# Optimization experiments

Measured on AMD Instinct MI355X. Metric: run time of the kernel, lower is better.

The kernel has to match this reference:

```python
import jax, jax.numpy as jnp
import numpy as np

B, C, H, W = 4, 256, 96, 96
HEADS, RATE = 8, 1


def setup_inputs() -> dict:
    key = jax.random.key(0)
    ks = [jax.random.fold_in(key, i) for i in range(8)]
    kpe = 2 * (RATE // 2) + 1  # PE depthwise kernel size (1 for rate=1)
    return {
        "q": jax.random.normal(ks[0], (B, C, H, W), jnp.float32),
        "k": jax.random.normal(ks[1], (B, C, H, W), jnp.float32),
        "v": jax.random.normal(ks[2], (B, C, H, W), jnp.float32),
        "wq": jax.random.normal(ks[3], (C, C), jnp.float32) * 0.02,          # q_proj 1x1 (used for q,k,v per source)
        "pe_dw": jax.random.normal(ks[4], (9, 1, kpe, kpe), jnp.float32) * 0.3,  # grouped conv, groups=9
        "pe_pw": jax.random.normal(ks[5], (9, 9, 1, 1), jnp.float32) * 0.3,      # 1x1 mixing conv
        "wo": jax.random.normal(ks[6], (C, C), jnp.float32) * 0.02,          # out_proj weight
        "bo": jax.random.normal(ks[7], (C,), jnp.float32) * 0.02,            # out_proj bias
    }


def _unfold3(x, rate):
    # torch.nn.Unfold(3, dilation=rate, padding=rate) then view(N, c, 9, H, W)
    # kernel positions are row-major (ki, kj), channel-major layout -> stack on axis 2.
    n, c, h, w = x.shape
    xp = jnp.pad(x, ((0, 0), (0, 0), (rate, rate), (rate, rate)))
    pats = [xp[:, :, i * rate:i * rate + h, j * rate:j * rate + w]
            for i in range(3) for j in range(3)]
    return jnp.stack(pats, axis=2)  # (N, c, 9, H, W)


def reference(q, b_unused_k=None, v=None, wq=None, pe_dw=None, pe_pw=None, wo=None, bo=None, k=None):
    raise NotImplementedError  # replaced below


def reference(q, k, v, wq, pe_dw, pe_pw, wo, bo):
    b = q.shape[0]
    ch = C // HEADS
    proj = lambda x: jnp.einsum('oc,bchw->bohw', wq, x)  # source uses q_proj for q, k AND v
    qh = proj(q).reshape(b * HEADS, ch, H, W)
    kh = proj(k).reshape(b * HEADS, ch, H, W)
    vh = proj(v).reshape(b * HEADS, ch, H, W)

    ku = _unfold3(kh, RATE)                              # (bH, ch, 9, H, W)
    f = jnp.einsum('nchw,nckhw->nkhw', qh, ku)           # per-pixel 3x3 scores (bH, 9, H, W)

    pad = RATE // 2
    dn = ('NCHW', 'OIHW', 'NCHW')
    f = jax.lax.conv_general_dilated(f, pe_dw, (1, 1), [(pad, pad), (pad, pad)],
                                     feature_group_count=9, dimension_numbers=dn)
    f = jax.lax.conv_general_dilated(f, pe_pw, (1, 1), 'VALID', dimension_numbers=dn)
    s = jax.nn.softmax(f, axis=1)                        # softmax over 9 kernel positions

    vu = _unfold3(vh, RATE)                              # (bH, ch, 9, H, W)
    o = jnp.einsum('nckhw,nkhw->nchw', vu, s).reshape(b, C, H, W)
    return jnp.einsum('oc,bchw->bohw', wo, o) + bo[None, :, None, None]
```

## Files before the change

### kernel.cpp

```cpp
#include <hip/hip_runtime.h>
#include <math.h>

#define HH 96
#define WW 96
#define PP 9216
#define CCH 256
#define BB 4
#define CH 32

typedef unsigned short u16;
typedef short bf16x8 __attribute__((ext_vector_type(8)));
typedef float f32x4 __attribute__((ext_vector_type(4)));

__device__ __forceinline__ float bf2f(unsigned s) { return __uint_as_float(s << 16); }
__device__ __forceinline__ u16 f2bf(float f) {
  unsigned u = __float_as_uint(f);
  return (u16)((u + 0x7fffu + ((u >> 16) & 1u)) >> 16);
}

typedef __attribute__((address_space(1))) const unsigned int GUI;
typedef __attribute__((address_space(3))) unsigned int LUI;
__device__ __forceinline__ void gload16(const void* g, void* l) {
  __builtin_amdgcn_global_load_lds((GUI*)g, (LUI*)l, 16, 0, 0);
}

__global__ __launch_bounds__(256)
void wcvt(const float* __restrict__ wq, const float* __restrict__ wo,
          u16* __restrict__ Wbf) {
  int gidx = blockIdx.x * 256 + threadIdx.x;
  int mat = gidx >> 13;
  int gi = gidx & 8191;
  int l = gi & 63;
  int i = (gi >> 6) & 3;
  int w = (gi >> 8) & 3;
  int ks = (gi >> 10) & 1;
  int kk = (gi >> 11) & 3;
  const float* W = mat ? wo : wq;
  int row = w * 64 + i * 16 + (l & 15);
  int c0 = kk * 64 + (ks * 4 + (l >> 4)) * 8;
  const float* s = W + (size_t)row * CCH + c0;
  float4 a = *(const float4*)s;
  float4 b = *(const float4*)(s + 4);
  uint4 u;
  u.x = (unsigned)f2bf(a.x) | ((unsigned)f2bf(a.y) << 16);
  u.y = (unsigned)f2bf(a.z) | ((unsigned)f2bf(a.w) << 16);
  u.z = (unsigned)f2bf(b.x) | ((unsigned)f2bf(b.y) << 16);
  u.w = (unsigned)f2bf(b.z) | ((unsigned)f2bf(b.w) << 16);
  *(uint4*)(Wbf + (size_t)gidx * 8) = u;
}

#define XROW 264
__global__ __launch_bounds__(512, 6)
void gemm_qkvf(const float* __restrict__ qin, const float* __restrict__ kin,
               const float* __restrict__ vin, const u16* __restrict__ Wbf,
               u16* __restrict__ Xcl) {
  __shared__ u16 Xb[64 * XROW];
  const int t = threadIdx.x;
  const int w = t >> 6, l = t & 63;
  const int lr = l & 15, lg = l >> 4;
  const int pblk = blockIdx.x * 64;
  const int z = blockIdx.z;
  const int b = z & 3, which = z >> 2;
  const float* Xf = ((which == 0) ? qin : (which == 1) ? kin : vin) + (size_t)b * CCH * PP;
  u16* Y = Xcl + (size_t)z * ((size_t)PP * CCH);

  float4 xr[8];
#pragma unroll
  for (int rr = 0; rr < 8; rr++) {
    int cc = w * 32 + rr * 4 + lg;
    xr[rr] = *(const float4*)(Xf + (size_t)cc * PP + pblk + lr * 4);
  }
#pragma unroll
  for (int rr = 0; rr < 8; rr++) {
    float r0 = xr[rr].x, r1 = xr[rr].y, r2 = xr[rr].z, r3 = xr[rr].w;
    bool b0 = (lg & 1), b1 = (lg & 2);
    float s0 = b0 ? r0 : r1;
    float s1 = b0 ? r2 : r3;
    float u0 = __shfl_xor(s0, 16, 64);
    float u1 = __shfl_xor(s1, 16, 64);
    float m0 = b0 ? u0 : r0;
    float m1 = b0 ? r1 : u0;
    float m2 = b0 ? u1 : r2;
    float m3 = b0 ? r3 : u1;
    float s2 = b1 ? m0 : m2;
    float s3 = b1 ? m1 : m3;
    float w0 = __shfl_xor(s2, 32, 64);
    float w1 = __shfl_xor(s3, 32, 64);
    float o0 = b1 ? w0 : m0;
    float o1 = b1 ? w1 : m1;
    float o2 = b1 ? m2 : w0;
    float o3 = b1 ? m3 : w1;
    int cbase = w * 32 + rr * 4;
    int pl = lr * 4 + lg;
    unsigned lo = (unsigned)f2bf(o0) | ((unsigned)f2bf(o1) << 16);
    unsigned hi = (unsigned)f2bf(o2) | ((unsigned)f2bf(o3) << 16);
    *(uint2*)(&Xb[pl * XROW + cbase]) = make_uint2(lo, hi);
  }
  __syncthreads();

  f32x4 acc[2][4];
#pragma unroll
  for (int mi = 0; mi < 2; mi++)
#pragma unroll
    for (int ni = 0; ni < 4; ni++) acc[mi][ni] = (f32x4){0.f, 0.f, 0.f, 0.f};

#pragma unroll
  for (int kk = 0; kk < 4; kk++)
#pragma unroll
    for (int ks = 0; ks < 2; ks++) {
      const int q = kk * 8 + ks * 4 + lg;
      bf16x8 wf[2], xf[4];
#pragma unroll
      for (int mi = 0; mi < 2; mi++) {
        size_t go = ((((size_t)(kk * 2 + ks) * 4 + (w >> 1)) * 4 +
                      ((w & 1) * 2 + mi)) * 64 + l) * 8;
        wf[mi] = *(const bf16x8*)(Wbf + go);
      }
#pragma unroll
      for (int i = 0; i < 4; i++) {
        int row = i * 16 + lr;
        xf[i] = *(const bf16x8*)&Xb[row * XROW + q * 8];
      }
#pragma unroll
      for (int mi = 0; mi < 2; mi++)
#pragma unroll
        for (int ni = 0; ni < 4; ni++)
          acc[mi][ni] = __builtin_amdgcn_mfma_f32_16x16x32_bf16(
              wf[mi], xf[ni], acc[mi][ni], 0, 0, 0);
    }

#pragma unroll
  for (int mi = 0; mi < 2; mi++)
#pragma unroll
    for (int ni = 0; ni < 4; ni++) {
      int o = w * 32 + mi * 16 + lg * 4;
      int p = pblk + ni * 16 + lr;
      f32x4 a = acc[mi][ni];
      uint2 u;
      u.x = (unsigned)f2bf(a[0]) | ((unsigned)f2bf(a[1]) << 16);
      u.y = (unsigned)f2bf(a[2]) | ((unsigned)f2bf(a[3]) << 16);
      *(uint2*)(Y + (size_t)p * CCH + o) = u;
    }
}

__global__ __launch_bounds__(256)
void gemm_out_m(const u16* __restrict__ Xbuf, const u16* __restrict__ Wbf,
                const float* __restrict__ bias, float* __restrict__ outY) {
  __shared__ u16 Xl[64 * 256];
  const int t = threadIdx.x;
  const int w = t >> 6, l = t & 63;
  const int lr = l & 15, lg = l >> 4;
  const int pblk = blockIdx.x * 64;
  const int z = blockIdx.z;
  const u16* Xb = Xbuf + (size_t)z * ((size_t)PP * CCH);

#pragma unroll
  for (int r = 0; r < 8; r++) {
    int G = r * 256 + t;
    int row = G >> 5, g = G & 31;
    int gs = (g & 24) | ((g & 7) ^ (row & 7));
    gload16(Xb + (size_t)(pblk + row) * CCH + gs * 8, (void*)&Xl[(size_t)G * 8]);
  }
  __syncthreads();

  f32x4 acc[4][4];
#pragma unroll
  for (int mi = 0; mi < 4; mi++)
#pragma unroll
    for (int ni = 0; ni < 4; ni++) acc[mi][ni] = (f32x4){0.f, 0.f, 0.f, 0.f};

#pragma unroll
  for (int kk = 0; kk < 4; kk++)
#pragma unroll
    for (int ks = 0; ks < 2; ks++) {
      const int q = kk * 8 + ks * 4 + lg;
      bf16x8 wf[4], xf[4];
#pragma unroll
      for (int i = 0; i < 4; i++) {
        size_t go = ((((size_t)(kk * 2 + ks) * 4 + w) * 4 + i) * 64 + l) * 8;
        wf[i] = *(const bf16x8*)(Wbf + go);
      }
#pragma unroll
      for (int i = 0; i < 4; i++) {
        int row = i * 16 + lr;
        int qp = (q & 24) | ((q & 7) ^ (row & 7));
        xf[i] = *(const bf16x8*)&Xl[row * 256 + qp * 8];
      }
#pragma unroll
      for (int mi = 0; mi < 4; mi++)
#pragma unroll
        for (int ni = 0; ni < 4; ni++)
          acc[mi][ni] = __builtin_amdgcn_mfma_f32_16x16x32_bf16(
              xf[mi], wf[ni], acc[mi][ni], 0, 0, 0);
    }

#pragma unroll
  for (int ni = 0; ni < 4; ni++) {
    int o = w * 64 + ni * 16 + lr;
    float bv = bias[o];
#pragma unroll
    for (int mi = 0; mi < 4; mi++) {
      int p = pblk + mi * 16 + lg * 4;
      f32x4 a = acc[mi][ni];
      float4 st = {a[0] + bv, a[1] + bv, a[2] + bv, a[3] + bv};
      *(float4*)(outY + ((size_t)z * CCH + o) * PP + p) = st;
    }
  }
}

#define TX 32
#define TY 4
#define HX 34
#define HY 6
#define NHP (HX * HY)
#define NGR (NHP * 4)
#define ARND 4

__device__ __forceinline__ void fma8(const uint4 u, const float* qp, float& s) {
  s = fmaf(qp[0], bf2f(u.x & 0xffffu), s);
  s = fmaf(qp[1], bf2f(u.x >> 16), s);
  s = fmaf(qp[2], bf2f(u.y & 0xffffu), s);
  s = fmaf(qp[3], bf2f(u.y >> 16), s);
  s = fmaf(qp[4], bf2f(u.z & 0xffffu), s);
  s = fmaf(qp[5], bf2f(u.z >> 16), s);
  s = fmaf(qp[6], bf2f(u.w & 0xffffu), s);
  s = fmaf(qp[7], bf2f(u.w >> 16), s);
}
__device__ __forceinline__ void acc8(const uint4 u, float gv, float* op) {
  op[0] = fmaf(gv, bf2f(u.x & 0xffffu), op[0]);
  op[1] = fmaf(gv, bf2f(u.x >> 16), op[1]);
  op[2] = fmaf(gv, bf2f(u.y & 0xffffu), op[2]);
  op[3] = fmaf(gv, bf2f(u.y >> 16), op[3]);
  op[4] = fmaf(gv, bf2f(u.z & 0xffffu), op[4]);
  op[5] = fmaf(gv, bf2f(u.z >> 16), op[5]);
  op[6] = fmaf(gv, bf2f(u.w & 0xffffu), op[6]);
  op[7] = fmaf(gv, bf2f(u.w >> 16), op[7]);
}

__global__ __launch_bounds__(256)
void attn_1b(const u16* __restrict__ Kt, const u16* __restrict__ Vt,
             u16* __restrict__ Qt, const float* __restrict__ pe_dw,
             const float* __restrict__ pe_pw) {
  __shared__ __align__(16) u16 kl[NHP * 32];
  __shared__ __align__(16) u16 vl[NHP * 32];
  __shared__ float coef[81];
  const int t = threadIdx.x;
  if (t < 81) coef[t] = pe_pw[t] * pe_dw[t % 9];

  const int lx = t & 31;
  const int h2 = (t >> 5) & 1;
  const int ly = t >> 6;
  const int x0 = blockIdx.x * TX;
  const int y0 = blockIdx.y * TY;
  const int b = blockIdx.z >> 3;
  const int h = blockIdx.z & 7;
  const size_t nbase = (size_t)b * PP * CCH + h * CH;
  const int p = (y0 + ly) * WW + (x0 + lx);
  const size_t pixhalf = nbase + (size_t)p * CCH + h2 * 16;

  uint4 kg[ARND], vg[ARND];
#pragma unroll
  for (int r = 0; r < ARND; r++) {
    int s = t + r * 256;
    int pix = s >> 2, g = s & 3;
    int hy = pix / HX, hx = pix - hy * HX;
    int gx = x0 - 1 + hx, gy = y0 - 1 + hy;
    bool ok = (s < NGR) & (gx >= 0) & (gx < WW) & (gy >= 0) & (gy < HH);
    uint4 u = make_uint4(0u, 0u, 0u, 0u);
    if (ok) u = *(const uint4*)(Kt + nbase + (size_t)(gy * WW + gx) * CCH + g * 8);
    kg[r] = u;
  }
#pragma unroll
  for (int r = 0; r < ARND; r++) {
    int s = t + r * 256;
    int pix = s >> 2, g = s & 3;
    int hy = pix / HX, hx = pix - hy * HX;
    int gx = x0 - 1 + hx, gy = y0 - 1 + hy;
    bool ok = (s < NGR) & (gx >= 0) & (gx < WW) & (gy >= 0) & (gy < HH);
    uint4 u = make_uint4(0u, 0u, 0u, 0u);
    if (ok) u = *(const uint4*)(Vt + nbase + (size_t)(gy * WW + gx) * CCH + g * 8);
    vg[r] = u;
  }
  uint4 q0 = *(const uint4*)(Qt + pixhalf);
  uint4 q1 = *(const uint4*)(Qt + pixhalf + 8);

#pragma unroll
  for (int r = 0; r < ARND; r++) {
    int s = t + r * 256;
    if (s < NGR) {
      int pix = s >> 2, g = s & 3;
      *(uint4*)(&kl[pix * 32 + (((g + (pix >> 1)) & 3) << 3)]) = kg[r];
    }
  }
#pragma unroll
  for (int r = 0; r < ARND; r++) {
    int s = t + r * 256;
    if (s < NGR) {
      int pix = s >> 2, g = s & 3;
      *(uint4*)(&vl[pix * 32 + (((g + (pix >> 1)) & 3) << 3)]) = vg[r];
    }
  }
  __syncthreads();

  float qh[16];
  qh[0] = bf2f(q0.x & 0xffffu); qh[1] = bf2f(q0.x >> 16);
  qh[2] = bf2f(q0.y & 0xffffu); qh[3] = bf2f(q0.y >> 16);
  qh[4] = bf2f(q0.z & 0xffffu); qh[5] = bf2f(q0.z >> 16);
  qh[6] = bf2f(q0.w & 0xffffu); qh[7] = bf2f(q0.w >> 16);
  qh[8] = bf2f(q1.x & 0xffffu); qh[9] = bf2f(q1.x >> 16);
  qh[10] = bf2f(q1.y & 0xffffu); qh[11] = bf2f(q1.y >> 16);
  qh[12] = bf2f(q1.z & 0xffffu); qh[13] = bf2f(q1.z >> 16);
  qh[14] = bf2f(q1.w & 0xffffu); qh[15] = bf2f(q1.w >> 16);

  float f[9];
#pragma unroll
  for (int kk = 0; kk < 9; kk++) {
    int pix = (ly + kk / 3) * HX + lx + kk % 3;
    int ga = h2 * 2;
    uint4 ka = *(const uint4*)(&kl[pix * 32 + (((ga + (pix >> 1)) & 3) << 3)]);
    uint4 kb = *(const uint4*)(&kl[pix * 32 + (((ga + 1 + (pix >> 1)) & 3) << 3)]);
    float s = 0.f;
    fma8(ka, qh, s);
    fma8(kb, qh + 8, s);
    f[kk] = s + __shfl_xor(s, 32, 64);
  }

  float g[9], m = -1e30f;
#pragma unroll
  for (int k2 = 0; k2 < 9; k2++) {
    float s = 0.f;
#pragma unroll
    for (int kk = 0; kk < 9; kk++) s = fmaf(coef[k2 * 9 + kk], f[kk], s);
    g[k2] = s;
    m = fmaxf(m, s);
  }
  float ssum = 0.f;
#pragma unroll
  for (int k2 = 0; k2 < 9; k2++) {
    g[k2] = __expf(g[k2] - m);
    ssum += g[k2];
  }
  float inv = 1.f / ssum;
#pragma unroll
  for (int k2 = 0; k2 < 9; k2++) g[k2] *= inv;

  float oh[16];
#pragma unroll
  for (int j = 0; j < 16; j++) oh[j] = 0.f;
#pragma unroll
  for (int kk = 0; kk < 9; kk++) {
    int pix = (ly + kk / 3) * HX + lx + kk % 3;
    int ga = h2 * 2;
    uint4 va = *(const uint4*)(&vl[pix * 32 + (((ga + (pix >> 1)) & 3) << 3)]);
    uint4 vb = *(const uint4*)(&vl[pix * 32 + (((ga + 1 + (pix >> 1)) & 3) << 3)]);
    acc8(va, g[kk], oh);
    acc8(vb, g[kk], oh + 8);
  }
  uint4 s0, s1;
  s0.x = (unsigned)f2bf(oh[0]) | ((unsigned)f2bf(oh[1]) << 16);
  s0.y = (unsigned)f2bf(oh[2]) | ((unsigned)f2bf(oh[3]) << 16);
  s0.z = (unsigned)f2bf(oh[4]) | ((unsigned)f2bf(oh[5]) << 16);
  s0.w = (unsigned)f2bf(oh[6]) | ((unsigned)f2bf(oh[7]) << 16);
  s1.x = (unsigned)f2bf(oh[8]) | ((unsigned)f2bf(oh[9]) << 16);
  s1.y = (unsigned)f2bf(oh[10]) | ((unsigned)f2bf(oh[11]) << 16);
  s1.z = (unsigned)f2bf(oh[12]) | ((unsigned)f2bf(oh[13]) << 16);
  s1.w = (unsigned)f2bf(oh[14]) | ((unsigned)f2bf(oh[15]) << 16);
  *(uint4*)(Qt + pixhalf) = s0;
  *(uint4*)(Qt + pixhalf + 8) = s1;
}

extern "C" void kernel_launch(void* const* d_in, const int* in_sizes, int n_in,
                              void* d_out, int out_size, void* d_ws, size_t ws_size,
                              hipStream_t stream) {
  const float* q     = (const float*)d_in[0];
  const float* k     = (const float*)d_in[1];
  const float* v     = (const float*)d_in[2];
  const float* wq    = (const float*)d_in[3];
  const float* pe_dw = (const float*)d_in[4];
  const float* pe_pw = (const float*)d_in[5];
  const float* wo    = (const float*)d_in[6];
  const float* bo    = (const float*)d_in[7];
  float* out = (float*)d_out;

  const size_t seg = (size_t)BB * PP * CCH;
  u16* Xcl = (u16*)d_ws;
  u16* Wbf = Xcl + 3 * seg;

  wcvt<<<64, 256, 0, stream>>>(wq, wo, Wbf);

  gemm_qkvf<<<dim3(PP / 64, 1, 12), 512, 0, stream>>>(q, k, v, Wbf, Xcl);

  u16* Qs = Xcl;
  u16* Ks = Xcl + seg;
  u16* Vs = Xcl + 2 * seg;
  attn_1b<<<dim3(WW / TX, HH / TY, BB * 8), 256, 0, stream>>>(Ks, Vs, Qs, pe_dw, pe_pw);

  gemm_out_m<<<dim3(PP / 64, 1, BB), 256, 0, stream>>>(Qs, Wbf + 65536, bo, out);
}
```

Measured before the change: 88.27 us.

## Stage fp32 activations via LDS DMA double buffer before bf16 transpose

The q/k/v projection GEMM no longer loads fp32 activations into registers and transposes them with cross-lane shuffles. It now issues global_load_lds copies into a double-buffered fp32 LDS tile, 64 channels at a time, then does the channel-to-pixel transpose and bf16 packing from LDS. The next chunk's load is issued while the current chunk is converted, to overlap memory traffic with conversion and remove shuffle work. In exchange, LDS use per block roughly doubles and the occupancy hint of 6 is dropped from launch bounds, which may lower occupancy. The loop also adds four extra block barriers.

```diff
diff --git a/kernel.cpp b/kernel.cpp
--- a/kernel.cpp
+++ b/kernel.cpp
@@ -50,10 +50,11 @@
 }
 
 #define XROW 264
-__global__ __launch_bounds__(512, 6)
+__global__ __launch_bounds__(512)
 void gemm_qkvf(const float* __restrict__ qin, const float* __restrict__ kin,
                const float* __restrict__ vin, const u16* __restrict__ Wbf,
                u16* __restrict__ Xcl) {
+  __shared__ float fA[2][64 * 64];
   __shared__ u16 Xb[64 * XROW];
   const int t = threadIdx.x;
   const int w = t >> 6, l = t & 63;
@@ -64,39 +65,37 @@
   const float* Xf = ((which == 0) ? qin : (which == 1) ? kin : vin) + (size_t)b * CCH * PP;
   u16* Y = Xcl + (size_t)z * ((size_t)PP * CCH);
 
-  float4 xr[8];
-#pragma unroll
-  for (int rr = 0; rr < 8; rr++) {
-    int cc = w * 32 + rr * 4 + lg;
-    xr[rr] = *(const float4*)(Xf + (size_t)cc * PP + pblk + lr * 4);
-  }
-#pragma unroll
-  for (int rr = 0; rr < 8; rr++) {
-    float r0 = xr[rr].x, r1 = xr[rr].y, r2 = xr[rr].z, r3 = xr[rr].w;
-    bool b0 = (lg & 1), b1 = (lg & 2);
-    float s0 = b0 ? r0 : r1;
-    float s1 = b0 ? r2 : r3;
-    float u0 = __shfl_xor(s0, 16, 64);
-    float u1 = __shfl_xor(s1, 16, 64);
-    float m0 = b0 ? u0 : r0;
-    float m1 = b0 ? r1 : u0;
-    float m2 = b0 ? u1 : r2;
-    float m3 = b0 ? r3 : u1;
-    float s2 = b1 ? m0 : m2;
-    float s3 = b1 ? m1 : m3;
-    float w0 = __shfl_xor(s2, 32, 64);
-    float w1 = __shfl_xor(s3, 32, 64);
-    float o0 = b1 ? w0 : m0;
-    float o1 = b1 ? w1 : m1;
-    float o2 = b1 ? m2 : w0;
-    float o3 = b1 ? m3 : w1;
-    int cbase = w * 32 + rr * 4;
-    int pl = lr * 4 + lg;
-    unsigned lo = (unsigned)f2bf(o0) | ((unsigned)f2bf(o1) << 16);
-    unsigned hi = (unsigned)f2bf(o2) | ((unsigned)f2bf(o3) << 16);
-    *(uint2*)(&Xb[pl * XROW + cbase]) = make_uint2(lo, hi);
-  }
+  auto stage = [&](int q, int buf) {
+#pragma unroll
+    for (int i = 0; i < 2; i++) {
+      int inst = w * 2 + i;
+      int c = q * 64 + inst * 4 + (l >> 4);
+      gload16(Xf + (size_t)c * PP + pblk + (l & 15) * 4,
+              (void*)&fA[buf][inst * 256]);
+    }
+  };
+  auto trans = [&](int q, int buf) {
+    const int gc = w;
+    const float* src = &fA[buf][gc * 8 * 64 + l];
+    unsigned wds[4];
+#pragma unroll
+    for (int j = 0; j < 4; j++) {
+      float e0 = src[(2 * j) * 64];
+      float e1 = src[(2 * j + 1) * 64];
+      wds[j] = (unsigned)f2bf(e0) | ((unsigned)f2bf(e1) << 16);
+    }
+    *(uint4*)(&Xb[l * XROW + (q * 8 + gc) * 8]) =
+        make_uint4(wds[0], wds[1], wds[2], wds[3]);
+  };
+
+  stage(0, 0);
   __syncthreads();
+#pragma unroll
+  for (int q = 0; q < 4; q++) {
+    if (q < 3) stage(q + 1, (q + 1) & 1);
+    trans(q, q & 1);
+    __syncthreads();
+  }
 
   f32x4 acc[2][4];
 #pragma unroll
@@ -108,7 +107,7 @@
   for (int kk = 0; kk < 4; kk++)
 #pragma unroll
     for (int ks = 0; ks < 2; ks++) {
-      const int q = kk * 8 + ks * 4 + lg;
+      const int qcol = kk * 8 + ks * 4 + lg;
       bf16x8 wf[2], xf[4];
 #pragma unroll
       for (int mi = 0; mi < 2; mi++) {
@@ -119,7 +118,7 @@
 #pragma unroll
       for (int i = 0; i < 4; i++) {
         int row = i * 16 + lr;
-        xf[i] = *(const bf16x8*)&Xb[row * XROW + q * 8];
+        xf[i] = *(const bf16x8*)&Xb[row * XROW + qcol * 8];
       }
 #pragma unroll
       for (int mi = 0; mi < 2; mi++)
```

Result: slower. 90.28 us (+2.3%).
